# Kernel tuning notes

Measured on AMD Instinct MI355X. Metric: run time of the kernel, lower is better.

Reference implementation:

```python
import jax, jax.numpy as jnp
import numpy as np

EMBED = 768
HEADS = 12
FACTOR = 2
LN_EPS = 1e-5


def layer_norm(x, gamma, beta):
    mu = jnp.mean(x, axis=-1, keepdims=True)
    var = jnp.mean(jnp.square(x - mu), axis=-1, keepdims=True)
    return (x - mu) * jax.lax.rsqrt(var + LN_EPS) * gamma + beta


def setup_inputs() -> dict:
    key = jax.random.key(0)
    ks = jax.random.split(key, 8)
    B, S, E = 8, 1024, EMBED
    H = FACTOR * E
    s_e = 1.0 / np.sqrt(E)
    s_h = 1.0 / np.sqrt(H)
    return {
        "x": jax.random.normal(ks[0], (B, S, E), jnp.float32),
        "Wq": jax.random.normal(ks[1], (E, E), jnp.float32) * s_e,
        "Wk": jax.random.normal(ks[2], (E, E), jnp.float32) * s_e,
        "Wv": jax.random.normal(ks[3], (E, E), jnp.float32) * s_e,
        "W1": jax.random.normal(ks[4], (E, H), jnp.float32) * s_e,
        "b1": jnp.zeros((H,), jnp.float32),
        "W2": jax.random.normal(ks[5], (H, E), jnp.float32) * s_h,
        "b2": jnp.zeros((E,), jnp.float32),
        "g1": jnp.ones((E,), jnp.float32),
        "beta1": jnp.zeros((E,), jnp.float32),
        "g2": jnp.ones((E,), jnp.float32),
        "beta2": jnp.zeros((E,), jnp.float32),
    }


def reference(x, Wq, Wk, Wv, W1, b1, W2, b2, g1, beta1, g2, beta2):
    B, S, E = x.shape
    hd = E // HEADS
    # NOTE: original reshapes (B,S,E)->(B,H,S,hd) WITHOUT transposing heads
    # (non-standard: mixes sequence blocks across heads) - replicated faithfully.
    q = (x @ Wq).reshape(B, HEADS, S, hd)
    k = (x @ Wk).reshape(B, HEADS, S, hd)
    v = (x @ Wv).reshape(B, HEADS, S, hd)
    # no 1/sqrt(d) scaling in the original
    attn = jax.nn.softmax(jnp.einsum('bnqd,bnkd->bnqk', q, k), axis=-1)
    # NOTE: original einsum 'bnqk,bnvd->bnqd' sums over BOTH k and v
    # (value is sum-pooled over its sequence axis) - replicated faithfully.
    out = jnp.einsum('bnqk,bnvd->bnqd', attn, v)
    out = out.transpose(0, 2, 1, 3).reshape(B, S, E)
    a = x + layer_norm(out, g1, beta1)
    # GELU after BOTH linears (exact GELU, torch default)
    h = jax.nn.gelu(a @ W1 + b1, approximate=False)
    m = jax.nn.gelu(h @ W2 + b2, approximate=False)
    return x + layer_norm(m, g2, beta2)
```

## Files before the change

### kernel.cpp

```cpp
#include <hip/hip_runtime.h>
#include <hip/hip_bf16.h>
#include <math.h>

#define E_ 768
#define HID_ 1536
#define SQ_ 1024

typedef unsigned short u16;
using bf16x8 = __attribute__((ext_vector_type(8))) __bf16;
using f32x16 = __attribute__((ext_vector_type(16))) float;

__device__ __forceinline__ u16 f2bf(float f) {
  union { float f; unsigned u; } v; v.f = f;
  unsigned r = v.u + 0x7FFFu + ((v.u >> 16) & 1u);
  return (u16)(r >> 16);
}
__device__ __forceinline__ float bf2f(u16 h) {
  union { unsigned u; float f; } v; v.u = ((unsigned)h) << 16; return v.f;
}
__device__ __forceinline__ float gelu_f(float x) {
  return 0.5f * x * (1.0f + erff(x * 0.70710678118654752f));
}

#define GLDS16(gp, sp) __builtin_amdgcn_global_load_lds( \
    (__attribute__((address_space(1))) const void*)(const void*)(gp), \
    (__attribute__((address_space(3))) void*)(void*)(sp), 16, 0, 0)

__global__ void prep_kernel(const float* __restrict__ x, const float* __restrict__ W1,
                            const float* __restrict__ W2, u16* __restrict__ xb,
                            u16* __restrict__ W1T, u16* __restrict__ W2T) {
  __shared__ float T[64 * 65];
  int bid = blockIdx.x, t = threadIdx.x;
  if (bid < 6144) {
    int base = bid * 1024 + t * 4;
    const float4 v = *reinterpret_cast<const float4*>(x + base);
    ushort4 o; o.x = f2bf(v.x); o.y = f2bf(v.y); o.z = f2bf(v.z); o.w = f2bf(v.w);
    *reinterpret_cast<ushort4*>(xb + base) = o;
    return;
  }
  const float* in; u16* out; int R_in, C_in, rt, ct;
  if (bid < 6432) {
    int b2 = bid - 6144; in = W1; out = W1T; R_in = 768; C_in = 1536;
    rt = b2 / 24; ct = b2 % 24;
  } else {
    int b3 = bid - 6432; in = W2; out = W2T; R_in = 1536; C_in = 768;
    rt = b3 / 12; ct = b3 % 12;
  }
  int r0 = rt << 6, c0 = ct << 6;
  int tr = t >> 4, tc4 = (t & 15) << 2;
#pragma unroll
  for (int i = 0; i < 4; ++i) {
    int row = tr + (i << 4);
    const float4 v = *reinterpret_cast<const float4*>(in + (size_t)(r0 + row) * C_in + c0 + tc4);
    T[row * 65 + tc4 + 0] = v.x;
    T[row * 65 + tc4 + 1] = v.y;
    T[row * 65 + tc4 + 2] = v.z;
    T[row * 65 + tc4 + 3] = v.w;
  }
  __syncthreads();
#pragma unroll
  for (int i = 0; i < 4; ++i) {
    int orow = tr + (i << 4);
    ushort4 o;
    o.x = f2bf(T[(tc4 + 0) * 65 + orow]);
    o.y = f2bf(T[(tc4 + 1) * 65 + orow]);
    o.z = f2bf(T[(tc4 + 2) * 65 + orow]);
    o.w = f2bf(T[(tc4 + 3) * 65 + orow]);
    *reinterpret_cast<ushort4*>(out + (size_t)(c0 + orow) * R_in + r0 + tc4) = o;
  }
}

__global__ void rowsum_kernel(const u16* __restrict__ xb, float* __restrict__ Rp) {
  int bid = blockIdx.x;
  int r = bid >> 2, c = bid & 3;
  int b = r / 12, n = r % 12;
  int t = threadIdx.x;
  int u0 = n << 10;
  int s_lo = u0 / 12;
  int s_hi = (u0 + 1023) / 12;
  int cnt = s_hi - s_lo + 1;
  int cs = s_lo + (cnt * c) / 4;
  int ce = s_lo + (cnt * (c + 1)) / 4;
  float acc[12][4];
#pragma unroll
  for (int g = 0; g < 12; ++g)
    for (int q = 0; q < 4; ++q) acc[g][q] = 0.f;
  const u16* xp = xb + (size_t)b * SQ_ * E_ + (t << 2);
  for (int s = cs; s < ce; ++s) {
    ushort4 vv = *reinterpret_cast<const ushort4*>(xp + (size_t)s * E_);
    float v0 = bf2f(vv.x), v1 = bf2f(vv.y), v2 = bf2f(vv.z), v3 = bf2f(vv.w);
    int du = 12 * s - u0;
#pragma unroll
    for (int g = 0; g < 12; ++g) {
      int u = du + g;
      if (u >= 0 && u < 1024) {
        acc[g][0] += v0; acc[g][1] += v1; acc[g][2] += v2; acc[g][3] += v3;
      }
    }
  }
  float* Rr = Rp + (size_t)bid * 9216 + (t << 2);
#pragma unroll
  for (int g = 0; g < 12; ++g) {
    float4 o; o.x = acc[g][0]; o.y = acc[g][1]; o.z = acc[g][2]; o.w = acc[g][3];
    *reinterpret_cast<float4*>(Rr + g * 768) = o;
  }
}

__global__ void ygemm_kernel(const float* __restrict__ Rp, const float* __restrict__ Wv,
                             float* __restrict__ P3) {
  int g = blockIdx.x, r = blockIdx.y, jc = blockIdx.z;
  int t = threadIdx.x;
  int d = t & 63, sub = t >> 6;
  const float* R0 = Rp + (size_t)r * 4 * 9216 + g * 768;
  const float* wp = Wv + g * 64 + d;
  int j0 = jc * 96 + sub * 24;
  float a0 = 0.f, a1 = 0.f, a2 = 0.f, a3 = 0.f;
#pragma unroll
  for (int jj = 0; jj < 24; jj += 4) {
    int j = j0 + jj;
    float r0v = R0[j + 0] + R0[9216 + j + 0] + R0[18432 + j + 0] + R0[27648 + j + 0];
    float r1v = R0[j + 1] + R0[9216 + j + 1] + R0[18432 + j + 1] + R0[27648 + j + 1];
    float r2v = R0[j + 2] + R0[9216 + j + 2] + R0[18432 + j + 2] + R0[27648 + j + 2];
    float r3v = R0[j + 3] + R0[9216 + j + 3] + R0[18432 + j + 3] + R0[27648 + j + 3];
    a0 += r0v * wp[(size_t)(j + 0) * 768];
    a1 += r1v * wp[(size_t)(j + 1) * 768];
    a2 += r2v * wp[(size_t)(j + 2) * 768];
    a3 += r3v * wp[(size_t)(j + 3) * 768];
  }
  __shared__ float red[256];
  red[t] = (a0 + a1) + (a2 + a3);
  __syncthreads();
  if (sub == 0)
    P3[(((size_t)r * 12 + g) * 8 + jc) * 64 + d] = red[d] + red[64 + d] + red[128 + d] + red[192 + d];
}

__global__ void ysum_kernel(const float* __restrict__ P3, float* __restrict__ Y) {
  int bn = blockIdx.x;
  int t = threadIdx.x;
  int d = t & 63, sub = t >> 6;
  const float* Pp = P3 + (size_t)bn * 6144 + d;
  int g0 = sub * 24;
  float s = 0.f;
#pragma unroll 8
  for (int gj = 0; gj < 24; ++gj) s += Pp[(g0 + gj) << 6];
  __shared__ float red[256];
  red[t] = s;
  __syncthreads();
  if (sub == 0)
    Y[bn * 64 + d] = red[d] + red[64 + d] + red[128 + d] + red[192 + d];
}

__global__ void c1_kernel(const float* __restrict__ Y, const float* __restrict__ W1,
                          const float* __restrict__ b1, const float* __restrict__ g1,
                          const float* __restrict__ be1, float* __restrict__ C1) {
  int bid = blockIdx.x;
  int b = bid / 48, c = bid % 48;
  int t = threadIdx.x;
  __shared__ float Ls[768];
  __shared__ float red2[8];
  __shared__ float red[8][32];
  float y0 = Y[b * 768 + t];
  float y1 = Y[b * 768 + t + 256];
  float y2 = Y[b * 768 + t + 512];
  float s = y0 + y1 + y2;
  float sq = y0 * y0 + y1 * y1 + y2 * y2;
#pragma unroll
  for (int o = 32; o > 0; o >>= 1) { s += __shfl_down(s, o, 64); sq += __shfl_down(sq, o, 64); }
  if ((t & 63) == 0) { red2[(t >> 6) * 2] = s; red2[(t >> 6) * 2 + 1] = sq; }
  __syncthreads();
  s  = red2[0] + red2[2] + red2[4] + red2[6];
  sq = red2[1] + red2[3] + red2[5] + red2[7];
  float mu = s * (1.f / 768.f);
  float var = sq * (1.f / 768.f) - mu * mu;
  float rs = rsqrtf(var + 1e-5f);
  Ls[t]       = (y0 - mu) * rs * g1[t]       + be1[t];
  Ls[t + 256] = (y1 - mu) * rs * g1[t + 256] + be1[t + 256];
  Ls[t + 512] = (y2 - mu) * rs * g1[t + 512] + be1[t + 512];
  __syncthreads();
  int tc = t & 31, ts = t >> 5;
  int n = c * 32 + tc;
  float acc = 0.f;
  int j0 = ts * 96;
#pragma unroll 4
  for (int j = j0; j < j0 + 96; ++j) acc += Ls[j] * W1[(size_t)j * HID_ + n];
  red[ts][tc] = acc;
  __syncthreads();
  if (ts == 0) {
    float sum = b1[n];
#pragma unroll
    for (int k = 0; k < 8; ++k) sum += red[k][tc];
    C1[b * HID_ + n] = sum;
  }
}

template <int MODE>
__global__ __launch_bounds__(256, 3) void gemm_bt_kernel(
    const u16* __restrict__ A, const u16* __restrict__ BT,
    const float* __restrict__ bias, void* __restrict__ out0, void* __restrict__ out1,
    int N, int lda, int ldb) {
  __shared__ __align__(16) u16 As[128 * 64];
  __shared__ __align__(16) u16 Bs[128 * 64];
  int bid = blockIdx.x;
  int xcd = bid & 7, idx = bid >> 3;
  int mloc, n_, k_off, kk = 0;
  if (MODE == 0) { mloc = idx / 12; n_ = idx % 12; k_off = 0; }
  else           { kk = idx / 48; int rem = idx % 48; mloc = rem / 6; n_ = rem % 6; k_off = kk * 768; }
  int bm = (xcd * 8 + mloc) << 7, bn = n_ << 7;

  int t = threadIdx.x;
  int lane = t & 63, w = t >> 6;
  int wm = (w >> 1) << 6, wn = (w & 1) << 6;
  int l32 = lane & 31, half = lane >> 5;
  f32x16 acc[2][2] = {};

  for (int k0 = 0; k0 < 768; k0 += 64) {
    __syncthreads();
#pragma unroll
    for (int i = 0; i < 4; ++i) {
      int ci = t + (i << 8);
      int r = ci >> 3, csw = ci & 7;
      int kc = csw ^ (r & 7);
      const u16* ga = A + (size_t)(bm + r) * lda + k_off + k0 + (kc << 3);
      GLDS16(ga, As + ci * 8);
      const u16* gb = BT + (size_t)(bn + r) * ldb + k_off + k0 + (kc << 3);
      GLDS16(gb, Bs + ci * 8);
    }
    __builtin_amdgcn_s_waitcnt(0);
    __syncthreads();
#pragma unroll
    for (int kc = 0; kc < 4; ++kc) {
      int kc2 = (kc << 1) | half;
      bf16x8 af[2], bf[2];
#pragma unroll
      for (int mt = 0; mt < 2; ++mt) {
        int row = wm + (mt << 5) + l32;
        af[mt] = *reinterpret_cast<const bf16x8*>(As + row * 64 + ((kc2 ^ (row & 7)) << 3));
      }
#pragma unroll
      for (int nt = 0; nt < 2; ++nt) {
        int row = wn + (nt << 5) + l32;
        bf[nt] = *reinterpret_cast<const bf16x8*>(Bs + row * 64 + ((kc2 ^ (row & 7)) << 3));
      }
#pragma unroll
      for (int mt = 0; mt < 2; ++mt)
#pragma unroll
        for (int nt = 0; nt < 2; ++nt)
          acc[mt][nt] = __builtin_amdgcn_mfma_f32_32x32x16_bf16(af[mt], bf[nt], acc[mt][nt], 0, 0, 0);
    }
  }

#pragma unroll
  for (int mt = 0; mt < 2; ++mt) {
    int rbase = bm + wm + (mt << 5) + (half << 2);
#pragma unroll
    for (int nt = 0; nt < 2; ++nt) {
      int col = bn + wn + (nt << 5) + l32;
      float bv = (MODE == 0) ? bias[(bm >> 10) * N + col] : 0.f;
#pragma unroll
      for (int reg = 0; reg < 16; ++reg) {
        int row = rbase + (reg & 3) + ((reg >> 2) << 3);
        float v = acc[mt][nt][reg] + bv;
        size_t idxo = (size_t)row * N + col;
        if (MODE == 0)       ((u16*)out0)[idxo] = f2bf(gelu_f(v));
        else if (kk == 0)    ((u16*)out0)[idxo] = f2bf(v);
        else                 ((u16*)out1)[idxo] = f2bf(v);
      }
    }
  }
}

__global__ void ln2_kernel(const u16* __restrict__ p0, const u16* __restrict__ p1,
                           const float* __restrict__ x, const float* __restrict__ b2,
                           const float* __restrict__ g2, const float* __restrict__ be2,
                           float* __restrict__ out) {
  int row = blockIdx.x, t = threadIdx.x;
  int e = t << 2;
  ushort4 pa = *reinterpret_cast<const ushort4*>(p0 + (size_t)row * 768 + e);
  ushort4 pb = *reinterpret_cast<const ushort4*>(p1 + (size_t)row * 768 + e);
  float4 bb = *reinterpret_cast<const float4*>(b2 + e);
  float v0 = gelu_f(bf2f(pa.x) + bf2f(pb.x) + bb.x);
  float v1 = gelu_f(bf2f(pa.y) + bf2f(pb.y) + bb.y);
  float v2 = gelu_f(bf2f(pa.z) + bf2f(pb.z) + bb.z);
  float v3 = gelu_f(bf2f(pa.w) + bf2f(pb.w) + bb.w);
  float s = (v0 + v1) + (v2 + v3);
  float sq = (v0 * v0 + v1 * v1) + (v2 * v2 + v3 * v3);
  __shared__ float red[6];
#pragma unroll
  for (int o = 32; o > 0; o >>= 1) { s += __shfl_down(s, o, 64); sq += __shfl_down(sq, o, 64); }
  if ((t & 63) == 0) { red[(t >> 6) * 2] = s; red[(t >> 6) * 2 + 1] = sq; }
  __syncthreads();
  s  = red[0] + red[2] + red[4];
  sq = red[1] + red[3] + red[5];
  float mu = s * (1.f / 768.f);
  float var = sq * (1.f / 768.f) - mu * mu;
  float rs = rsqrtf(var + 1e-5f);
  float4 gg = *reinterpret_cast<const float4*>(g2 + e);
  float4 be = *reinterpret_cast<const float4*>(be2 + e);
  float4 xx = *reinterpret_cast<const float4*>(x + (size_t)row * 768 + e);
  float4 o;
  o.x = xx.x + (v0 - mu) * rs * gg.x + be.x;
  o.y = xx.y + (v1 - mu) * rs * gg.y + be.y;
  o.z = xx.z + (v2 - mu) * rs * gg.z + be.z;
  o.w = xx.w + (v3 - mu) * rs * gg.w + be.w;
  *reinterpret_cast<float4*>(out + (size_t)row * 768 + e) = o;
}

extern "C" void kernel_launch(void* const* d_in, const int* in_sizes, int n_in,
                              void* d_out, int out_size, void* d_ws, size_t ws_size,
                              hipStream_t stream) {
  const float* x   = (const float*)d_in[0];
  const float* Wv  = (const float*)d_in[3];
  const float* W1  = (const float*)d_in[4];
  const float* b1  = (const float*)d_in[5];
  const float* W2  = (const float*)d_in[6];
  const float* b2  = (const float*)d_in[7];
  const float* g1  = (const float*)d_in[8];
  const float* be1 = (const float*)d_in[9];
  const float* g2  = (const float*)d_in[10];
  const float* be2 = (const float*)d_in[11];
  float* out = (float*)d_out;

  char* ws = (char*)d_ws;
  u16*   xb  = (u16*)(ws);
  u16*   W1T = (u16*)(ws + 12582912);
  u16*   W2T = (u16*)(ws + 14942208);
  u16*   h   = (u16*)(ws + 17301504);
  float* Rp  = (float*)(ws + 17301504);
  float* P3  = (float*)(ws + 42467328);
  float* Y   = (float*)(ws + 44826624);
  float* C1  = (float*)(ws + 44875776);
  u16*   m0  = (u16*)(ws + 44924928);
  u16*   p1  = xb;

  prep_kernel<<<6720, 256, 0, stream>>>(x, W1, W2, xb, W1T, W2T);
  rowsum_kernel<<<384, 192, 0, stream>>>(xb, Rp);
  ygemm_kernel<<<dim3(12, 96, 8), 256, 0, stream>>>(Rp, Wv, P3);
  ysum_kernel<<<96, 256, 0, stream>>>(P3, Y);
  c1_kernel<<<384, 256, 0, stream>>>(Y, W1, b1, g1, be1, C1);
  gemm_bt_kernel<0><<<768, 256, 0, stream>>>(xb, W1T, C1, (void*)h, nullptr, 1536, 768, 768);
  gemm_bt_kernel<1><<<768, 256, 0, stream>>>(h, W2T, nullptr, (void*)m0, (void*)p1, 768, 1536, 1536);
  ln2_kernel<<<8192, 192, 0, stream>>>(m0, p1, x, b2, g2, be2, out);
}
```

Measured before the change: 243.8 us.

## Fuse ysum into ygemm via atomics, switch GEMM to 16x16 MFMA, read bf16 residual

The separate ysum pass is removed: ygemm now atomically accumulates its partial sums into Y, which an extra prep block zeroes first. The bf16 GEMM moves from 32x32x16 MFMA tiles to 16x16x32 tiles with a 4x4 accumulator grid and launch bounds lowered from 3 to 2 waves. The final LayerNorm reads the bf16 copy of x for the residual instead of fp32 to cut memory traffic. To keep xb valid for that read, p1 gets its own workspace region. Risks are atomic contention, lower occupancy, and a less precise residual that could exceed tolerance.

```diff
diff --git a/kernel.cpp b/kernel.cpp
--- a/kernel.cpp
+++ b/kernel.cpp
@@ -8,7 +8,7 @@
 
 typedef unsigned short u16;
 using bf16x8 = __attribute__((ext_vector_type(8))) __bf16;
-using f32x16 = __attribute__((ext_vector_type(16))) float;
+using f32x4  = __attribute__((ext_vector_type(4))) float;
 
 __device__ __forceinline__ u16 f2bf(float f) {
   union { float f; unsigned u; } v; v.f = f;
@@ -28,9 +28,17 @@
 
 __global__ void prep_kernel(const float* __restrict__ x, const float* __restrict__ W1,
                             const float* __restrict__ W2, u16* __restrict__ xb,
-                            u16* __restrict__ W1T, u16* __restrict__ W2T) {
+                            u16* __restrict__ W1T, u16* __restrict__ W2T,
+                            float* __restrict__ Y) {
   __shared__ float T[64 * 65];
   int bid = blockIdx.x, t = threadIdx.x;
+  if (bid == 6720) {
+    float4 z = {0.f, 0.f, 0.f, 0.f};
+#pragma unroll
+    for (int i = 0; i < 6; ++i)
+      *reinterpret_cast<float4*>(Y + (i * 256 + t) * 4) = z;
+    return;
+  }
   if (bid < 6144) {
     int base = bid * 1024 + t * 4;
     const float4 v = *reinterpret_cast<const float4*>(x + base);
@@ -107,7 +115,7 @@
 }
 
 __global__ void ygemm_kernel(const float* __restrict__ Rp, const float* __restrict__ Wv,
-                             float* __restrict__ P3) {
+                             float* __restrict__ Y) {
   int g = blockIdx.x, r = blockIdx.y, jc = blockIdx.z;
   int t = threadIdx.x;
   int d = t & 63, sub = t >> 6;
@@ -131,23 +139,7 @@
   red[t] = (a0 + a1) + (a2 + a3);
   __syncthreads();
   if (sub == 0)
-    P3[(((size_t)r * 12 + g) * 8 + jc) * 64 + d] = red[d] + red[64 + d] + red[128 + d] + red[192 + d];
-}
-
-__global__ void ysum_kernel(const float* __restrict__ P3, float* __restrict__ Y) {
-  int bn = blockIdx.x;
-  int t = threadIdx.x;
-  int d = t & 63, sub = t >> 6;
-  const float* Pp = P3 + (size_t)bn * 6144 + d;
-  int g0 = sub * 24;
-  float s = 0.f;
-#pragma unroll 8
-  for (int gj = 0; gj < 24; ++gj) s += Pp[(g0 + gj) << 6];
-  __shared__ float red[256];
-  red[t] = s;
-  __syncthreads();
-  if (sub == 0)
-    Y[bn * 64 + d] = red[d] + red[64 + d] + red[128 + d] + red[192 + d];
+    atomicAdd(&Y[r * 64 + d], red[d] + red[64 + d] + red[128 + d] + red[192 + d]);
 }
 
 __global__ void c1_kernel(const float* __restrict__ Y, const float* __restrict__ W1,
@@ -194,7 +186,7 @@
 }
 
 template <int MODE>
-__global__ __launch_bounds__(256, 3) void gemm_bt_kernel(
+__global__ __launch_bounds__(256, 2) void gemm_bt_kernel(
     const u16* __restrict__ A, const u16* __restrict__ BT,
     const float* __restrict__ bias, void* __restrict__ out0, void* __restrict__ out1,
     int N, int lda, int ldb) {
@@ -210,8 +202,8 @@
   int t = threadIdx.x;
   int lane = t & 63, w = t >> 6;
   int wm = (w >> 1) << 6, wn = (w & 1) << 6;
-  int l32 = lane & 31, half = lane >> 5;
-  f32x16 acc[2][2] = {};
+  int quad = lane >> 4, l16 = lane & 15;
+  f32x4 acc[4][4] = {};
 
   for (int k0 = 0; k0 < 768; k0 += 64) {
     __syncthreads();
@@ -228,39 +220,38 @@
     __builtin_amdgcn_s_waitcnt(0);
     __syncthreads();
 #pragma unroll
-    for (int kc = 0; kc < 4; ++kc) {
-      int kc2 = (kc << 1) | half;
-      bf16x8 af[2], bf[2];
-#pragma unroll
-      for (int mt = 0; mt < 2; ++mt) {
-        int row = wm + (mt << 5) + l32;
-        af[mt] = *reinterpret_cast<const bf16x8*>(As + row * 64 + ((kc2 ^ (row & 7)) << 3));
+    for (int ks = 0; ks < 2; ++ks) {
+      bf16x8 af[4], bf[4];
+      int kc = (ks << 2) + quad;
+#pragma unroll
+      for (int mt = 0; mt < 4; ++mt) {
+        int row = wm + (mt << 4) + l16;
+        af[mt] = *reinterpret_cast<const bf16x8*>(As + row * 64 + ((kc ^ (row & 7)) << 3));
       }
 #pragma unroll
-      for (int nt = 0; nt < 2; ++nt) {
-        int row = wn + (nt << 5) + l32;
-        bf[nt] = *reinterpret_cast<const bf16x8*>(Bs + row * 64 + ((kc2 ^ (row & 7)) << 3));
+      for (int nt = 0; nt < 4; ++nt) {
+        int row = wn + (nt << 4) + l16;
+        bf[nt] = *reinterpret_cast<const bf16x8*>(Bs + row * 64 + ((kc ^ (row & 7)) << 3));
       }
 #pragma unroll
-      for (int mt = 0; mt < 2; ++mt)
-#pragma unroll
-        for (int nt = 0; nt < 2; ++nt)
-          acc[mt][nt] = __builtin_amdgcn_mfma_f32_32x32x16_bf16(af[mt], bf[nt], acc[mt][nt], 0, 0, 0);
+      for (int mt = 0; mt < 4; ++mt)
+#pragma unroll
+        for (int nt = 0; nt < 4; ++nt)
+          acc[mt][nt] = __builtin_amdgcn_mfma_f32_16x16x32_bf16(af[mt], bf[nt], acc[mt][nt], 0, 0, 0);
     }
   }
 
 #pragma unroll
-  for (int mt = 0; mt < 2; ++mt) {
-    int rbase = bm + wm + (mt << 5) + (half << 2);
-#pragma unroll
-    for (int nt = 0; nt < 2; ++nt) {
-      int col = bn + wn + (nt << 5) + l32;
+  for (int mt = 0; mt < 4; ++mt) {
+    int row0 = bm + wm + (mt << 4) + (quad << 2);
+#pragma unroll
+    for (int nt = 0; nt < 4; ++nt) {
+      int col = bn + wn + (nt << 4) + l16;
       float bv = (MODE == 0) ? bias[(bm >> 10) * N + col] : 0.f;
 #pragma unroll
-      for (int reg = 0; reg < 16; ++reg) {
-        int row = rbase + (reg & 3) + ((reg >> 2) << 3);
-        float v = acc[mt][nt][reg] + bv;
-        size_t idxo = (size_t)row * N + col;
+      for (int rr = 0; rr < 4; ++rr) {
+        float v = acc[mt][nt][rr] + bv;
+        size_t idxo = (size_t)(row0 + rr) * N + col;
         if (MODE == 0)       ((u16*)out0)[idxo] = f2bf(gelu_f(v));
         else if (kk == 0)    ((u16*)out0)[idxo] = f2bf(v);
         else                 ((u16*)out1)[idxo] = f2bf(v);
@@ -270,7 +261,7 @@
 }
 
 __global__ void ln2_kernel(const u16* __restrict__ p0, const u16* __restrict__ p1,
-                           const float* __restrict__ x, const float* __restrict__ b2,
+                           const u16* __restrict__ xb, const float* __restrict__ b2,
                            const float* __restrict__ g2, const float* __restrict__ be2,
                            float* __restrict__ out) {
   int row = blockIdx.x, t = threadIdx.x;
@@ -296,12 +287,12 @@
   float rs = rsqrtf(var + 1e-5f);
   float4 gg = *reinterpret_cast<const float4*>(g2 + e);
   float4 be = *reinterpret_cast<const float4*>(be2 + e);
-  float4 xx = *reinterpret_cast<const float4*>(x + (size_t)row * 768 + e);
+  ushort4 xx = *reinterpret_cast<const ushort4*>(xb + (size_t)row * 768 + e);
   float4 o;
-  o.x = xx.x + (v0 - mu) * rs * gg.x + be.x;
-  o.y = xx.y + (v1 - mu) * rs * gg.y + be.y;
-  o.z = xx.z + (v2 - mu) * rs * gg.z + be.z;
-  o.w = xx.w + (v3 - mu) * rs * gg.w + be.w;
+  o.x = bf2f(xx.x) + (v0 - mu) * rs * gg.x + be.x;
+  o.y = bf2f(xx.y) + (v1 - mu) * rs * gg.y + be.y;
+  o.z = bf2f(xx.z) + (v2 - mu) * rs * gg.z + be.z;
+  o.w = bf2f(xx.w) + (v3 - mu) * rs * gg.w + be.w;
   *reinterpret_cast<float4*>(out + (size_t)row * 768 + e) = o;
 }
 
@@ -326,18 +317,16 @@
   u16*   W2T = (u16*)(ws + 14942208);
   u16*   h   = (u16*)(ws + 17301504);
   float* Rp  = (float*)(ws + 17301504);
-  float* P3  = (float*)(ws + 42467328);
   float* Y   = (float*)(ws + 44826624);
   float* C1  = (float*)(ws + 44875776);
   u16*   m0  = (u16*)(ws + 44924928);
-  u16*   p1  = xb;
-
-  prep_kernel<<<6720, 256, 0, stream>>>(x, W1, W2, xb, W1T, W2T);
+  u16*   p1  = (u16*)(ws + 57507840);
+
+  prep_kernel<<<6721, 256, 0, stream>>>(x, W1, W2, xb, W1T, W2T, Y);
   rowsum_kernel<<<384, 192, 0, stream>>>(xb, Rp);
-  ygemm_kernel<<<dim3(12, 96, 8), 256, 0, stream>>>(Rp, Wv, P3);
-  ysum_kernel<<<96, 256, 0, stream>>>(P3, Y);
+  ygemm_kernel<<<dim3(12, 96, 8), 256, 0, stream>>>(Rp, Wv, Y);
   c1_kernel<<<384, 256, 0, stream>>>(Y, W1, b1, g1, be1, C1);
   gemm_bt_kernel<0><<<768, 256, 0, stream>>>(xb, W1T, C1, (void*)h, nullptr, 1536, 768, 768);
   gemm_bt_kernel<1><<<768, 256, 0, stream>>>(h, W2T, nullptr, (void*)m0, (void*)p1, 768, 1536, 1536);
-  ln2_kernel<<<8192, 192, 0, stream>>>(m0, p1, x, b2, g2, be2, out);
-}
+  ln2_kernel<<<8192, 192, 0, stream>>>(m0, p1, xb, b2, g2, be2, out);
+}
```

New measurement: 241.5 us. Within noise of the previous version (-1.0%).
